# Kernel tuning notes

Hardware: AMD Instinct MI355X
Metric: run time of the kernel (lower is better)

## Reference

```python
import jax, jax.numpy as jnp
import numpy as np

B, T, F_, S, H = 4096, 128, 96, 128, 512
IMPUTE_WEIGHT = 0.3
L1, L2 = 0.01, 0.1


def setup_inputs() -> dict:
    key = jax.random.key(0)
    ks = jax.random.split(key, 28)
    def n(k, shape, s=0.05):
        return jax.random.normal(k, shape, jnp.float32) * s
    return dict(
        values=jax.random.normal(ks[0], (B, T, F_), jnp.float32),
        masks=jax.random.bernoulli(ks[1], 0.8, (B, T, F_)).astype(jnp.float32),
        deltas=jax.random.uniform(ks[2], (B, T, F_), jnp.float32, 0.0, 5.0),
        statics=jax.random.normal(ks[3], (B, S), jnp.float32),
        static_masks=jax.random.bernoulli(ks[4], 0.8, (B, S)).astype(jnp.float32),
        labels=jax.random.bernoulli(ks[5], 0.5, (B,)).astype(jnp.float32),
        fr_W=n(ks[6], (S, S)), fr_b=n(ks[7], (S,)),
        d1_W=n(ks[8], (H, S)), d1_b=n(ks[9], (H,)),
        d2_W=n(ks[10], (H, H)), d2_b=n(ks[11], (H,)),
        d3_W=n(ks[12], (H, H)), d3_b=n(ks[13], (H,)),
        td_W=n(ks[14], (H, F_)), td_b=n(ks[15], (H,)),
        hist_W=n(ks[16], (F_, H)), hist_b=n(ks[17], (F_,)),
        st_W=n(ks[18], (F_, S)), st_b=n(ks[19], (F_,)),
        real_W=n(ks[20], (F_, F_)), real_b=n(ks[21], (F_,)),
        lstm_Wih=n(ks[22], (4 * H, 2 * F_)), lstm_Whh=n(ks[23], (4 * H, H)),
        lstm_bih=n(ks[24], (4 * H,)), lstm_bhh=n(ks[25], (4 * H,)),
        out_W=n(ks[26], (1, H)), out_b=n(ks[27], (1,)),
    )


def reference(values, masks, deltas, statics, static_masks, labels,
              fr_W, fr_b, d1_W, d1_b, d2_W, d2_b, d3_W, d3_b,
              td_W, td_b, hist_W, hist_b, st_W, st_b, real_W, real_b,
              lstm_Wih, lstm_Whh, lstm_bih, lstm_bhh, out_W, out_b):
    sg = jax.lax.stop_gradient
    # ---- MultiModal (dropout = identity in inference) ----
    s_h = statics @ fr_W.T + fr_b
    s_c = static_masks * statics + (1.0 - static_masks) * s_h
    s_tc = s_c
    s_loss = jnp.sum(jnp.abs(statics - s_c) * static_masks) / (jnp.sum(static_masks) + 1e-5)
    s_loss = s_loss + IMPUTE_WEIGHT * L2 * jnp.sum(jnp.abs(jnp.diagonal(sg(fr_W))))
    h = jax.nn.relu(s_c @ d1_W.T + d1_b)
    h = jax.nn.relu(h @ d2_W.T + d2_b)
    h = jax.nn.relu(h @ d3_W.T + d3_b)                 # initial hidden state
    c = jnp.zeros((values.shape[0], H), values.dtype)
    st_term = s_tc @ st_W.T + st_b

    def step(carry, xs):
        h, c, xl = carry
        x, m, d = xs                                   # each [B, F_]
        gamma = jnp.exp(-jax.nn.relu(d @ td_W.T + td_b))
        h = h * gamma
        x_c = (x @ real_W.T + real_b) + (h @ hist_W.T + hist_b) + st_term
        xl = xl + jnp.sum(jnp.abs(x - x_c) * m) / (jnp.sum(m) + 1e-5)
        c_c = m * x + (1.0 - m) * x_c
        inp = jnp.concatenate([c_c, m], axis=1)        # [B, 2*F_]
        gates = inp @ lstm_Wih.T + lstm_bih + h @ lstm_Whh.T + lstm_bhh
        i, f, g, o = jnp.split(gates, 4, axis=1)       # torch LSTMCell gate order
        c = jax.nn.sigmoid(f) * c + jax.nn.sigmoid(i) * jnp.tanh(g)
        h = jax.nn.sigmoid(o) * jnp.tanh(c)
        return (h, c, xl), c_c

    xs = (jnp.swapaxes(values, 0, 1), jnp.swapaxes(masks, 0, 1), jnp.swapaxes(deltas, 0, 1))
    (h, c, x_loss), imps = jax.lax.scan(step, (h, c, jnp.float32(0.0)), xs)
    imputations = jnp.swapaxes(imps, 0, 1)             # [B, T, F_]

    y_h = h @ out_W.T + out_b                          # [B, 1]
    z = y_h[:, 0]
    # BCE with logits, mean reduction (stable form)
    y_loss = jnp.mean(jnp.maximum(z, 0.0) - z * labels + jnp.log1p(jnp.exp(-jnp.abs(z))))
    # regularizers on .data (stop-gradient in torch semantics)
    r_loss = L1 * (jnp.sum(jnp.abs(sg(real_W))) + jnp.sum(jnp.abs(sg(hist_W))) + jnp.sum(jnp.abs(sg(st_W))))
    r_loss = r_loss + L2 * jnp.sum(jnp.abs(jnp.diagonal(sg(real_W))))
    loss = y_loss + r_loss + IMPUTE_WEIGHT * x_loss + s_loss
    return (loss, jax.nn.sigmoid(y_h), imputations)
```

## Files before the change

kernel.cpp:

```cpp
#include <hip/hip_runtime.h>
#include <math.h>

#define Bn 4096
#define Tn 128
#define Fn 96
#define Sn 128
#define Hn 512

typedef __attribute__((ext_vector_type(8))) short bf16x8;
typedef __attribute__((ext_vector_type(4))) float f32x4;

#define GC(p) ((const __attribute__((address_space(1))) void*)(p))
#define LC(p) ((__attribute__((address_space(3))) void*)(p))

__device__ __forceinline__ short tobf(float f){
  unsigned u = __float_as_uint(f);
  unsigned r = (u + 0x7fffu + ((u>>16)&1u)) >> 16;
  return (short)r;
}
__device__ __forceinline__ float bf2f(short s){
  return __uint_as_float(((unsigned)(unsigned short)s)<<16);
}
__device__ __forceinline__ float sigmf_(float x){ return 1.0f/(1.0f+expf(-x)); }

__device__ __forceinline__ int haddr(int row, int k){
  int c = k & 63;
  return ((k>>6)<<10) + (row<<6) + ((((c>>3) ^ (row&7)))<<3) + (c&7);
}

__device__ __forceinline__ void stage_tile(const short* gsrc, size_t sstride, int k0,
                                           short* lt, int rows, int wid, int lane, int nw){
  int calls = rows >> 3;
  for (int c = wid; c < calls; c += nw){
    int r = (c<<3) + (lane>>3);
    int ch = (lane&7) ^ (r&7);
    const short* gp = gsrc + (size_t)r*sstride + k0 + (ch<<3);
    __builtin_amdgcn_global_load_lds(GC(gp), LC(lt + (c<<9)), 16, 0, 0);
  }
}
__device__ __forceinline__ bf16x8 frag(const short* lt, int row, int ch){
  return *(const bf16x8*)(lt + (row<<6) + ((ch ^ (row&7))<<3));
}


__global__ void k_pack_td(const float* __restrict__ tdW, short* __restrict__ tdWp){
  int i = blockIdx.x*256 + threadIdx.x;
  if (i >= 512*128) return;
  int n = i>>7, k = i&127;
  tdWp[i] = (k < Fn) ? tobf(tdW[n*Fn + k]) : (short)0;
}
__global__ void k_pack_x(const float* __restrict__ realW, const float* __restrict__ histW,
                         const float* __restrict__ realb, const float* __restrict__ histb,
                         short* __restrict__ Wxp, float* __restrict__ bxp){
  int i = blockIdx.x*256 + threadIdx.x;
  if (i < Fn) bxp[i] = realb[i] + histb[i];
  if (i >= Fn*640) return;
  int f = i/640, k = i - f*640;
  float v = 0.f;
  if (k < 512) v = histW[f*Hn + k];
  else if (k < 608) v = realW[f*Fn + (k-512)];
  Wxp[i] = tobf(v);
}
__global__ void k_pack_g(const float* __restrict__ Wih, const float* __restrict__ Whh,
                         const float* __restrict__ bih, const float* __restrict__ bhh,
                         short* __restrict__ Wgp, float* __restrict__ bgp){
  int i = blockIdx.x*256 + threadIdx.x;
  if (i >= 16*128*704) return;
  int k = i % 704; int nc = i / 704;
  int pb = nc >> 7, ncol = nc & 127;
  int jj = pb*32 + (ncol >> 2), g = ncol & 3;
  int n = g*Hn + jj;
  float v;
  if (k < 512) v = Whh[(size_t)n*Hn + k];
  else if (k < 608) v = Wih[(size_t)n*192 + (k-512)];
  else v = Wih[(size_t)n*192 + 96 + (k-608)];
  Wgp[i] = tobf(v);
  if (k == 0) bgp[nc] = bih[n] + bhh[n];
}
__global__ void k_cvt(const float* __restrict__ src, short* __restrict__ dst, int n){
  int i = blockIdx.x*256 + threadIdx.x;
  if (i < n) dst[i] = tobf(src[i]);
}


__global__ void k_static(const float* __restrict__ statics, const float* __restrict__ smask,
                         const float* __restrict__ frW, const float* __restrict__ frb,
                         float* __restrict__ s_c){
  __shared__ float row[Sn];
  int b = blockIdx.x, j = threadIdx.x;
  row[j] = statics[b*Sn + j];
  __syncthreads();
  float acc = frb[j];
  #pragma unroll 4
  for (int k = 0; k < Sn; k++) acc += row[k] * frW[j*Sn + k];
  float m = smask[b*Sn + j];
  s_c[b*Sn + j] = m * row[j] + (1.0f - m) * acc;
}

template<int K, bool RELU, bool WF32>
__global__ __launch_bounds__(512) void k_gemm(const short* __restrict__ A,
    const short* __restrict__ B, const float* __restrict__ bias,
    short* __restrict__ outb, float* __restrict__ outf){
  __shared__ __align__(16) short stA[2][8192], stB[2][8192];
  const int tid = threadIdx.x, lane = tid&63, wid = tid>>6;
  const int mb = blockIdx.x >> 2, nb = blockIdx.x & 3;
  const int r0 = mb*128, c0 = nb*128;
  const int wM = wid>>1, wN = wid&1, lr = lane&15, lq = lane>>4;
  f32x4 acc[2][4];
  #pragma unroll
  for (int m=0;m<2;m++)
    #pragma unroll
    for (int n=0;n<4;n++) acc[m][n] = (f32x4){0,0,0,0};
  constexpr int NS = K/64;
  stage_tile(A + (size_t)r0*K, K, 0, stA[0], 128, wid, lane, 8);
  stage_tile(B + (size_t)c0*K, K, 0, stB[0], 128, wid, lane, 8);
  __syncthreads();
  for (int kc=0; kc<NS; kc++){
    if (kc < NS-1){
      stage_tile(A + (size_t)r0*K, K, (kc+1)*64, stA[(kc+1)&1], 128, wid, lane, 8);
      stage_tile(B + (size_t)c0*K, K, (kc+1)*64, stB[(kc+1)&1], 128, wid, lane, 8);
    }
    #pragma unroll
    for (int kk=0;kk<2;kk++){
      int ch = (kk<<2) + lq;
      bf16x8 af[2];
      #pragma unroll
      for (int m=0;m<2;m++) af[m] = frag(stA[kc&1], wM*32 + m*16 + lr, ch);
      #pragma unroll
      for (int n=0;n<4;n++){
        bf16x8 bf = frag(stB[kc&1], wN*64 + n*16 + lr, ch);
        #pragma unroll
        for (int m=0;m<2;m++)
          acc[m][n] = __builtin_amdgcn_mfma_f32_16x16x32_bf16(af[m], bf, acc[m][n],0,0,0);
      }
    }
    __syncthreads();
  }
  #pragma unroll
  for (int m=0;m<2;m++)
    #pragma unroll
    for (int n=0;n<4;n++){
      int col = c0 + wN*64 + n*16 + lr;
      float bv = bias[col];
      #pragma unroll
      for (int reg=0;reg<4;reg++){
        int row = r0 + wM*32 + m*16 + (lq<<2) + reg;
        float v = acc[m][n][reg] + bv;
        if (RELU) v = fmaxf(v, 0.f);
        outb[(size_t)row*512 + col] = tobf(v);
        if (WF32) outf[(size_t)row*512 + col] = v;
      }
    }
}

template<int K, int N, bool RELU>
__global__ void k_mlp(const float* __restrict__ in, const float* __restrict__ W,
                      const float* __restrict__ bias, float* __restrict__ out){
  __shared__ float row[K];
  int b = blockIdx.x;
  for (int i = threadIdx.x; i < K; i += blockDim.x) row[i] = in[b*K + i];
  __syncthreads();
  for (int n = threadIdx.x; n < N; n += blockDim.x){
    float acc = bias[n];
    #pragma unroll 4
    for (int k = 0; k < K; k++) acc += row[k] * W[n*K + k];
    if (RELU) acc = fmaxf(acc, 0.0f);
    out[b*N + n] = acc;
  }
}

__global__ void k_masksum(const float* __restrict__ masks, float* __restrict__ den){
  int t = blockIdx.x, tid = threadIdx.x;
  float s = 0.f;
  for (int i = tid; i < Bn*Fn; i += 256){
    int b = i / Fn, f = i - b*Fn;
    s += masks[((size_t)b*Tn + t)*Fn + f];
  }
  __shared__ float red[256];
  red[tid] = s; __syncthreads();
  for (int o = 128; o > 0; o >>= 1){ if (tid < o) red[tid] += red[tid + o]; __syncthreads(); }
  if (tid == 0) den[t] = red[0];
}

__global__ __launch_bounds__(512) void k_dxc(int t,
    const float* __restrict__ values, const float* __restrict__ masks,
    const float* __restrict__ deltas,
    const short* __restrict__ tdWp, const float* __restrict__ tdb,
    const short* __restrict__ Wxp,  const float* __restrict__ bxp,
    const float* __restrict__ st,   const float* __restrict__ h_g,
    short* __restrict__ inp, float* __restrict__ out_imp, float* __restrict__ num){
  __shared__ __align__(16) short Adel[2*1024];
  __shared__ __align__(16) short A2[10*1024];
  __shared__ short sm[16*96];
  __shared__ __align__(16) short Bst[2][8192];
  __shared__ float wred[8];
  const int tid = threadIdx.x, lane = tid&63, wid = tid>>6;
  const int r0 = blockIdx.x*16;
  const int lr = lane&15, lq = lane>>4;

  stage_tile(tdWp, 128, 0, Bst[0], 128, wid, lane, 8);

  if (tid < 384){
    int r = tid/24, fq = tid - r*24, f0 = fq*4;
    size_t gb = ((size_t)(r0+r)*Tn + t)*Fn + f0;
    float4 xv4 = *(const float4*)(values + gb);
    float4 mv4 = *(const float4*)(masks  + gb);
    float4 dv4 = *(const float4*)(deltas + gb);
    #pragma unroll
    for (int j=0;j<4;j++){
      int f = f0 + j;
      float xv = ((const float*)&xv4)[j];
      float mv = ((const float*)&mv4)[j];
      float dv = ((const float*)&dv4)[j];
      sm[r*96 + f] = tobf(mv);
      inp[(size_t)(r0+r)*704 + 608 + f] = tobf(mv);
      A2 [haddr(r, 512+f)] = tobf(xv);
      Adel[haddr(r, f)]    = tobf(dv);
    }
  }
  {
    int r = tid>>5, cz = tid&31;
    Adel[haddr(r,  96+cz)] = 0;
    A2  [haddr(r, 608+cz)] = 0;
  }
  __syncthreads();

  f32x4 accd[4];
  #pragma unroll
  for (int q=0;q<4;q++) accd[q] = (f32x4){0,0,0,0};
  for (int s=0; s<8; s++){
    int nq = s>>1, kc = s&1;
    if (s < 7){
      int s2 = s+1;
      stage_tile(tdWp + (size_t)((s2>>1)*128)*128, 128, (s2&1)*64, Bst[s2&1], 128, wid, lane, 8);
    } else {
      stage_tile(Wxp, 640, 0, Bst[0], 96, wid, lane, 8);
    }
    #pragma unroll
    for (int kk=0;kk<2;kk++){
      int ch = (kk<<2) + lq;
      bf16x8 af = frag(Adel + kc*1024, lr, ch);
      bf16x8 bf = frag(Bst[s&1], wid*16 + lr, ch);
      accd[nq] = __builtin_amdgcn_mfma_f32_16x16x32_bf16(af, bf, accd[nq], 0,0,0);
    }
    __syncthreads();
  }
  #pragma unroll
  for (int nq=0;nq<4;nq++){
    int col = nq*128 + wid*16 + lr;
    float tb = tdb[col];
    #pragma unroll
    for (int reg=0;reg<4;reg++){
      int row = (lq<<2) + reg;
      float v = accd[nq][reg] + tb;
      float hd = h_g[(size_t)(r0+row)*Hn + col] * __expf(-fmaxf(v,0.f));
      A2[haddr(row, col)] = tobf(hd);
      inp[(size_t)(r0+row)*704 + col] = tobf(hd);
    }
  }
  __syncthreads();

  f32x4 accx = (f32x4){0,0,0,0};
  for (int kx=0; kx<10; kx++){
    if (kx < 9) stage_tile(Wxp, 640, (kx+1)*64, Bst[(kx+1)&1], 96, wid, lane, 8);
    if (wid < 6){
      #pragma unroll
      for (int kk=0;kk<2;kk++){
        int ch = (kk<<2) + lq;
        bf16x8 af = frag(A2 + kx*1024, lr, ch);
        bf16x8 bf = frag(Bst[kx&1], wid*16 + lr, ch);
        accx = __builtin_amdgcn_mfma_f32_16x16x32_bf16(af, bf, accx, 0,0,0);
      }
    }
    __syncthreads();
  }
  float lsum = 0.f;
  if (wid < 6){
    int f = wid*16 + lr;
    float bx = bxp[f];
    #pragma unroll
    for (int reg=0;reg<4;reg++){
      int row = (lq<<2) + reg;
      float xcv = accx[reg] + bx + st[(size_t)(r0+row)*Fn + f];
      float xv = bf2f(A2[haddr(row, 512+f)]);
      float mv = bf2f(sm[row*96 + f]);
      lsum += fabsf(xv - xcv)*mv;
      float cc = mv*xv + (1.f-mv)*xcv;
      inp[(size_t)(r0+row)*704 + 512 + f] = tobf(cc);
      out_imp[((size_t)(r0+row)*Tn + t)*Fn + f] = cc;
    }
  }
  #pragma unroll
  for (int o=32;o>0;o>>=1) lsum += __shfl_down(lsum, o);
  if (lane==0) wred[wid] = lsum;
  __syncthreads();
  if (tid==0){
    float s2 = 0.f;
    #pragma unroll
    for (int w2=0;w2<8;w2++) s2 += wred[w2];
    atomicAdd(&num[t], s2);
  }
}

__global__ __launch_bounds__(512, 4) void k_gates(int t, const short* __restrict__ inp,
    const short* __restrict__ Wgp, const float* __restrict__ bgp,
    float* __restrict__ h_g, float* __restrict__ c_g){
  __shared__ __align__(16) short stA[2][8192], stB[2][8192];
  const int tid = threadIdx.x, lane = tid&63, wid = tid>>6;
  const int mb = blockIdx.x & 31, pb = blockIdx.x >> 5;
  const int r0 = mb*128;
  const short* gA = inp + (size_t)r0*704;
  const short* gB = Wgp + (size_t)pb*128*704;
  const int wM = wid>>1, wN = wid&1, lr = lane&15, lq = lane>>4;
  f32x4 acc[2][4];
  #pragma unroll
  for (int m=0;m<2;m++)
    #pragma unroll
    for (int n=0;n<4;n++) acc[m][n] = (f32x4){0,0,0,0};

  stage_tile(gA, 704, 0, stA[0], 128, wid, lane, 8);
  stage_tile(gB, 704, 0, stB[0], 128, wid, lane, 8);
  __syncthreads();

  for (int kc=0; kc<11; kc++){
    if (kc < 10){
      stage_tile(gA, 704, (kc+1)*64, stA[(kc+1)&1], 128, wid, lane, 8);
      stage_tile(gB, 704, (kc+1)*64, stB[(kc+1)&1], 128, wid, lane, 8);
    }
    #pragma unroll
    for (int kk=0;kk<2;kk++){
      int ch = (kk<<2) + lq;
      bf16x8 af[2];
      #pragma unroll
      for (int m=0;m<2;m++) af[m] = frag(stA[kc&1], wM*32 + m*16 + lr, ch);
      #pragma unroll
      for (int n=0;n<4;n++){
        bf16x8 bf = frag(stB[kc&1], wN*64 + n*16 + lr, ch);
        #pragma unroll
        for (int m=0;m<2;m++)
          acc[m][n] = __builtin_amdgcn_mfma_f32_16x16x32_bf16(af[m], bf, acc[m][n],0,0,0);
      }
    }
    __syncthreads();
  }

  const int g = lane&3;
  const float s_  = (g==2) ? 2.0f : -1.0f;
  const float ca_ = (g==2) ? -2.0f : 1.0f;
  const float cb_ = (g==2) ? 1.0f : 0.0f;
  #pragma unroll
  for (int m=0;m<2;m++){
    int row = r0 + wM*32 + m*16 + (lq<<2) + g;
    #pragma unroll
    for (int n=0;n<4;n++){
      int colbase = wN*64 + n*16 + lr;
      float b = bgp[pb*128 + colbase];
      float q0 = 1.f/(1.f+__expf(s_*(acc[m][n][0]+b))); float a0 = q0*ca_+cb_;
      float q1 = 1.f/(1.f+__expf(s_*(acc[m][n][1]+b))); float a1 = q1*ca_+cb_;
      float q2 = 1.f/(1.f+__expf(s_*(acc[m][n][2]+b))); float a2 = q2*ca_+cb_;
      float q3 = 1.f/(1.f+__expf(s_*(acc[m][n][3]+b))); float a3 = q3*ca_+cb_;
      int i1=g^1, i2=g^2, i3=g^3;
      float p1 = (i1==0)?a0:(i1==1)?a1:(i1==2)?a2:a3;
      float p2 = (i2==0)?a0:(i2==1)?a1:(i2==2)?a2:a3;
      float p3 = (i3==0)?a0:(i3==1)?a1:(i3==2)?a2:a3;
      float ow = (g==0)?a0:(g==1)?a1:(g==2)?a2:a3;
      float t1 = __shfl_xor(p1, 1, 64);
      float t2 = __shfl_xor(p2, 2, 64);
      float t3 = __shfl_xor(p3, 3, 64);
      float si = (g==0)?ow:(g==1)?t1:(g==2)?t2:t3;
      float sf = (g==1)?ow:(g==0)?t1:(g==3)?t2:t3;
      float tg = (g==2)?ow:(g==3)?t1:(g==0)?t2:t3;
      float so = (g==3)?ow:(g==2)?t1:(g==1)?t2:t3;
      int jh = pb*32 + (colbase>>2);
      size_t idx = (size_t)row*Hn + jh;
      float co = c_g[idx];
      float cn = sf*co + si*tg;
      float targ = fminf(fmaxf(2.0f*cn,-60.f),60.f);
      float e = __expf(targ); float th = (e-1.f)/(e+1.f);
      c_g[idx] = cn;
      h_g[idx] = so*th;
    }
  }
}


__global__ void k_out(const float* __restrict__ h_g, const float* __restrict__ outW,
                      const float* __restrict__ outb, const float* __restrict__ labels,
                      float* __restrict__ out_sig, float* __restrict__ yacc){
  int b = blockIdx.x, lane = threadIdx.x;
  float s = 0.f;
  for (int k = lane; k < Hn; k += 64) s += h_g[(size_t)b*Hn + k] * outW[k];
  #pragma unroll
  for (int o = 32; o > 0; o >>= 1) s += __shfl_down(s, o);
  if (lane == 0){
    float z = s + outb[0];
    out_sig[b] = sigmf_(z);
    float yl = fmaxf(z, 0.f) - z*labels[b] + log1pf(expf(-fabsf(z)));
    atomicAdd(yacc, yl);
  }
}

__global__ void k_loss(const float* __restrict__ realW, const float* __restrict__ histW,
                       const float* __restrict__ stW,   const float* __restrict__ frW,
                       const float* __restrict__ num,   const float* __restrict__ den,
                       const float* __restrict__ yacc,  float* __restrict__ out0){
  int tid = threadIdx.x;
  float r1 = 0.f;
  for (int i = tid; i < Fn*Fn; i += 256) r1 += fabsf(realW[i]);
  for (int i = tid; i < Fn*Hn; i += 256) r1 += fabsf(histW[i]);
  for (int i = tid; i < Fn*Sn; i += 256) r1 += fabsf(stW[i]);
  float rd = 0.f;
  for (int i = tid; i < Fn; i += 256) rd += fabsf(realW[i*Fn + i]);
  float fd = 0.f;
  for (int i = tid; i < Sn; i += 256) fd += fabsf(frW[i*Sn + i]);
  float xl = 0.f;
  for (int t = tid; t < Tn; t += 256) xl += num[t] / (den[t] + 1e-5f);
  float v = 0.01f*r1 + 0.1f*rd + 0.3f*xl + 0.03f*fd;
  __shared__ float red[256];
  red[tid] = v; __syncthreads();
  for (int o = 128; o > 0; o >>= 1){ if (tid < o) red[tid] += red[tid + o]; __syncthreads(); }
  if (tid == 0) out0[0] = red[0] + yacc[0] / (float)Bn;
}


extern "C" void kernel_launch(void* const* d_in, const int* in_sizes, int n_in,
                              void* d_out, int out_size, void* d_ws, size_t ws_size,
                              hipStream_t stream){
  const float* values = (const float*)d_in[0];
  const float* masks  = (const float*)d_in[1];
  const float* deltas = (const float*)d_in[2];
  const float* statics= (const float*)d_in[3];
  const float* smask  = (const float*)d_in[4];
  const float* labels = (const float*)d_in[5];
  const float* frW = (const float*)d_in[6];
  const float* frb = (const float*)d_in[7];
  const float* d1W = (const float*)d_in[8];
  const float* d1b = (const float*)d_in[9];
  const float* d2W = (const float*)d_in[10];
  const float* d2b = (const float*)d_in[11];
  const float* d3W = (const float*)d_in[12];
  const float* d3b = (const float*)d_in[13];
  const float* tdW = (const float*)d_in[14];
  const float* tdb = (const float*)d_in[15];
  const float* histW = (const float*)d_in[16];
  const float* histb = (const float*)d_in[17];
  const float* stW = (const float*)d_in[18];
  const float* stb = (const float*)d_in[19];
  const float* realW = (const float*)d_in[20];
  const float* realb = (const float*)d_in[21];
  const float* Wih = (const float*)d_in[22];
  const float* Whh = (const float*)d_in[23];
  const float* bih = (const float*)d_in[24];
  const float* bhh = (const float*)d_in[25];
  const float* outW = (const float*)d_in[26];
  const float* outb = (const float*)d_in[27];

  float* out0    = (float*)d_out;
  float* out_sig = out0 + 1;
  float* out_imp = out0 + 1 + Bn;

  float* wsf  = (float*)d_ws;
  float* s_c  = wsf;  wsf += Bn*Sn;
  float* h    = wsf;  wsf += (size_t)Bn*Hn;
  float* c    = wsf;  wsf += (size_t)Bn*Hn;
  float* st   = wsf;  wsf += Bn*Fn;
  float* den  = wsf;  wsf += Tn;
  float* num  = wsf;  wsf += Tn;
  float* yacc = num + Tn;
  wsf += 1;
  float* bxp  = wsf;  wsf += 128;
  float* bgp  = wsf;  wsf += 2048;
  size_t off = ((size_t)(wsf - (float*)d_ws) + 3u) & ~(size_t)3u;
  short* wss  = (short*)((float*)d_ws + off);
  short* tdWp = wss;  wss += 512*128;
  short* Wxp  = wss;  wss += 96*640;
  short* Wgp  = wss;  wss += (size_t)16*128*704;
  short* inp  = wss;  wss += (size_t)Bn*704;
  short* wd1  = wss;  wss += 512*128;
  short* wd2  = wss;  wss += 512*512;
  short* wd3  = wss;  wss += 512*512;
  short* act0 = wss;  wss += (size_t)Bn*128;
  short* actA = wss;  wss += (size_t)Bn*512;
  short* actB = wss;  wss += (size_t)Bn*512;

  hipMemsetAsync(c,   0, (size_t)Bn*Hn*sizeof(float), stream);
  hipMemsetAsync(num, 0, (Tn + 1)*sizeof(float), stream);

  k_pack_td<<<(512*128+255)/256, 256, 0, stream>>>(tdW, tdWp);
  k_pack_x <<<(96*640+255)/256, 256, 0, stream>>>(realW, histW, realb, histb, Wxp, bxp);
  k_pack_g <<<(16*128*704+255)/256, 256, 0, stream>>>(Wih, Whh, bih, bhh, Wgp, bgp);
  k_cvt<<<(512*128+255)/256, 256, 0, stream>>>(d1W, wd1, 512*128);
  k_cvt<<<(512*512+255)/256, 256, 0, stream>>>(d2W, wd2, 512*512);
  k_cvt<<<(512*512+255)/256, 256, 0, stream>>>(d3W, wd3, 512*512);

  k_static<<<Bn, Sn, 0, stream>>>(statics, smask, frW, frb, s_c);
  k_cvt<<<(Bn*Sn+255)/256, 256, 0, stream>>>(s_c, act0, Bn*Sn);
  k_gemm<128, true,  false><<<128, 512, 0, stream>>>(act0, wd1, d1b, actA, (float*)nullptr);
  k_gemm<512, true,  false><<<128, 512, 0, stream>>>(actA, wd2, d2b, actB, (float*)nullptr);
  k_gemm<512, true,  true ><<<128, 512, 0, stream>>>(actB, wd3, d3b, actA, h);
  k_mlp<Sn, Fn, false><<<Bn, 256, 0, stream>>>(s_c, stW, stb, st);
  k_masksum<<<Tn, 256, 0, stream>>>(masks, den);

  for (int t = 0; t < Tn; t++){
    k_dxc  <<<Bn/16,       512, 0, stream>>>(t, values, masks, deltas, tdWp, tdb,
                                             Wxp, bxp, st, h, inp, out_imp, num);
    k_gates<<<(Bn/128)*16, 512, 0, stream>>>(t, inp, Wgp, bgp, h, c);
  }

  k_out<<<Bn, 64, 0, stream>>>(h, outW, outb, labels, out_sig, yacc);
  k_loss<<<1, 256, 0, stream>>>(realW, histW, stW, frW, num, den, yacc, out0);
}
```

Before: 6.389 ms.

## Stage all decay and regression weight tiles into LDS upfront, dropping per-step barriers

Replaces the two-slot double buffer for the temporal-decay and feature-regression weight tiles in k_dxc with one large LDS buffer. All eight decay tiles are issued at once, overlapping the per-row input loads, and all ten regression tiles are issued right after the decay MFMAs. This removes the per-iteration __syncthreads and the serialized prefetch chain from both inner loops, and lets those loops fully unroll. In exchange LDS use per block rises to most of the CU's capacity, which limits the kernel to one resident block per CU.

```diff
diff --git a/kernel.cpp b/kernel.cpp
--- a/kernel.cpp
+++ b/kernel.cpp
@@ -192,30 +192,40 @@
   __shared__ __align__(16) short Adel[2*1024];
   __shared__ __align__(16) short A2[10*1024];
   __shared__ short sm[16*96];
-  __shared__ __align__(16) short Bst[2][8192];
+  __shared__ __align__(16) short Bbig[65536];
   __shared__ float wred[8];
   const int tid = threadIdx.x, lane = tid&63, wid = tid>>6;
   const int r0 = blockIdx.x*16;
   const int lr = lane&15, lq = lane>>4;
 
-  stage_tile(tdWp, 128, 0, Bst[0], 128, wid, lane, 8);
-
-  if (tid < 384){
-    int r = tid/24, fq = tid - r*24, f0 = fq*4;
-    size_t gb = ((size_t)(r0+r)*Tn + t)*Fn + f0;
-    float4 xv4 = *(const float4*)(values + gb);
-    float4 mv4 = *(const float4*)(masks  + gb);
-    float4 dv4 = *(const float4*)(deltas + gb);
+  float4 xv4, mv4, dv4;
+  const bool act = tid < 384;
+  int ar=0, af0=0;
+  if (act){
+    ar = tid/24; int fq = tid - ar*24; af0 = fq*4;
+    size_t gb = ((size_t)(r0+ar)*Tn + t)*Fn + af0;
+    xv4 = *(const float4*)(values + gb);
+    mv4 = *(const float4*)(masks  + gb);
+    dv4 = *(const float4*)(deltas + gb);
+  }
+
+  #pragma unroll
+  for (int s=0; s<8; s++){
+    int nq = s>>1, kc = s&1;
+    stage_tile(tdWp + (size_t)(nq*128)*128, 128, kc*64, Bbig + s*8192, 128, wid, lane, 8);
+  }
+
+  if (act){
     #pragma unroll
     for (int j=0;j<4;j++){
-      int f = f0 + j;
+      int f = af0 + j;
       float xv = ((const float*)&xv4)[j];
       float mv = ((const float*)&mv4)[j];
       float dv = ((const float*)&dv4)[j];
-      sm[r*96 + f] = tobf(mv);
-      inp[(size_t)(r0+r)*704 + 608 + f] = tobf(mv);
-      A2 [haddr(r, 512+f)] = tobf(xv);
-      Adel[haddr(r, f)]    = tobf(dv);
+      sm[ar*96 + f] = tobf(mv);
+      inp[(size_t)(r0+ar)*704 + 608 + f] = tobf(mv);
+      A2 [haddr(ar, 512+f)] = tobf(xv);
+      Adel[haddr(ar, f)]    = tobf(dv);
     }
   }
   {
@@ -228,23 +238,23 @@
   f32x4 accd[4];
   #pragma unroll
   for (int q=0;q<4;q++) accd[q] = (f32x4){0,0,0,0};
+  #pragma unroll
   for (int s=0; s<8; s++){
     int nq = s>>1, kc = s&1;
-    if (s < 7){
-      int s2 = s+1;
-      stage_tile(tdWp + (size_t)((s2>>1)*128)*128, 128, (s2&1)*64, Bst[s2&1], 128, wid, lane, 8);
-    } else {
-      stage_tile(Wxp, 640, 0, Bst[0], 96, wid, lane, 8);
-    }
     #pragma unroll
     for (int kk=0;kk<2;kk++){
       int ch = (kk<<2) + lq;
-      bf16x8 af = frag(Adel + kc*1024, lr, ch);
-      bf16x8 bf = frag(Bst[s&1], wid*16 + lr, ch);
-      accd[nq] = __builtin_amdgcn_mfma_f32_16x16x32_bf16(af, bf, accd[nq], 0,0,0);
-    }
-    __syncthreads();
-  }
+      bf16x8 afr = frag(Adel + kc*1024, lr, ch);
+      bf16x8 bfr = frag(Bbig + s*8192, wid*16 + lr, ch);
+      accd[nq] = __builtin_amdgcn_mfma_f32_16x16x32_bf16(afr, bfr, accd[nq], 0,0,0);
+    }
+  }
+  __syncthreads();
+
+  #pragma unroll
+  for (int kx=0; kx<10; kx++)
+    stage_tile(Wxp, 640, kx*64, Bbig + kx*6144, 96, wid, lane, 8);
+
   #pragma unroll
   for (int nq=0;nq<4;nq++){
     int col = nq*128 + wid*16 + lr;
@@ -261,18 +271,16 @@
   __syncthreads();
 
   f32x4 accx = (f32x4){0,0,0,0};
-  for (int kx=0; kx<10; kx++){
-    if (kx < 9) stage_tile(Wxp, 640, (kx+1)*64, Bst[(kx+1)&1], 96, wid, lane, 8);
-    if (wid < 6){
+  if (wid < 6){
+    #pragma unroll
+    for (int kx=0; kx<10; kx++)
       #pragma unroll
       for (int kk=0;kk<2;kk++){
         int ch = (kk<<2) + lq;
-        bf16x8 af = frag(A2 + kx*1024, lr, ch);
-        bf16x8 bf = frag(Bst[kx&1], wid*16 + lr, ch);
-        accx = __builtin_amdgcn_mfma_f32_16x16x32_bf16(af, bf, accx, 0,0,0);
+        bf16x8 afr = frag(A2 + kx*1024, lr, ch);
+        bf16x8 bfr = frag(Bbig + kx*6144, wid*16 + lr, ch);
+        accx = __builtin_amdgcn_mfma_f32_16x16x32_bf16(afr, bfr, accx, 0,0,0);
       }
-    }
-    __syncthreads();
   }
   float lsum = 0.f;
   if (wid < 6){
```

Result: faster. 5.999 ms (-6.1%).
